# Performance work log

Hardware: AMD Instinct MI355X
Metric: run time of the kernel (lower is better)

Reference implementation:

```python
import jax, jax.numpy as jnp
import numpy as np

NEG_SLOPE = 0.2   # PyG GATConv default negative_slope
BN_EPS = 1e-5
N_NODES = 50000
N_EDGES = 600000
N_GRAPHS = 64


def _gat_conv(x, W, att_src, att_dst, bias, src, dst, heads, out_ch, concat):
    """PyG GATConv (eval mode, self-loops already appended to src/dst).
    x: [N, in], W: [in, heads*out_ch], att_*: [heads, out_ch], bias: [heads*out_ch] or [out_ch].
    """
    n = x.shape[0]
    h = (x @ W).reshape(n, heads, out_ch)                  # [N, H, C]
    a_s = jnp.sum(h * att_src[None], axis=-1)              # [N, H]
    a_d = jnp.sum(h * att_dst[None], axis=-1)              # [N, H]
    logit = jax.nn.leaky_relu(a_s[src] + a_d[dst], NEG_SLOPE)  # [E, H]
    # segment softmax over destination node (every node has a self-loop -> no empty segment)
    m = jax.ops.segment_max(logit, dst, num_segments=n)
    p = jnp.exp(logit - m[dst])
    denom = jax.ops.segment_sum(p, dst, num_segments=n)
    alpha = p / (denom[dst] + 1e-16)                       # [E, H]
    out = jax.ops.segment_sum(h[src] * alpha[:, :, None], dst, num_segments=n)  # [N, H, C]
    out = out.reshape(n, heads * out_ch) if concat else out.mean(axis=1)
    return out + bias


def _bn(x, gamma, beta):
    mu = x.mean(axis=0)
    var = x.var(axis=0)
    return (x - mu) * jax.lax.rsqrt(var + BN_EPS) * gamma + beta


def setup_inputs() -> dict:
    key = jax.random.key(0)
    ks = jax.random.split(key, 20)
    hidden = 64
    d1_in, d1_out, h1 = 5, hidden // 2, 4          # 5 -> 32x4 = 128
    d2_in, d2_out, h2 = hidden * 2, hidden // 2, 4  # 128 -> 32x4 = 128
    d3_in, d3_out, h3 = hidden * 2, hidden, 1       # 128 -> 64

    def glorot(k, shape):
        fan = shape[0] + shape[-1]
        return jax.random.normal(k, shape, dtype=jnp.float32) * np.sqrt(2.0 / fan)

    inp = {
        "x": jax.random.normal(ks[0], (N_NODES, d1_in), dtype=jnp.float32),
        "edge_index": jax.random.randint(ks[1], (2, N_EDGES), 0, N_NODES),
        "batch": jnp.sort(jax.random.randint(ks[2], (N_NODES,), 0, N_GRAPHS)),
        # conv1
        "W1": glorot(ks[3], (d1_in, h1 * d1_out)),
        "a1_src": glorot(ks[4], (h1, d1_out)),
        "a1_dst": glorot(ks[5], (h1, d1_out)),
        "b1": jnp.zeros((h1 * d1_out,), dtype=jnp.float32),
        "g1": jnp.ones((h1 * d1_out,), dtype=jnp.float32),
        "be1": jnp.zeros((h1 * d1_out,), dtype=jnp.float32),
        # conv2
        "W2": glorot(ks[6], (d2_in, h2 * d2_out)),
        "a2_src": glorot(ks[7], (h2, d2_out)),
        "a2_dst": glorot(ks[8], (h2, d2_out)),
        "b2": jnp.zeros((h2 * d2_out,), dtype=jnp.float32),
        "g2": jnp.ones((h2 * d2_out,), dtype=jnp.float32),
        "be2": jnp.zeros((h2 * d2_out,), dtype=jnp.float32),
        # conv3 (single head, concat=False)
        "W3": glorot(ks[9], (d3_in, h3 * d3_out)),
        "a3_src": glorot(ks[10], (h3, d3_out)),
        "a3_dst": glorot(ks[11], (h3, d3_out)),
        "b3": jnp.zeros((d3_out,), dtype=jnp.float32),
    }
    return inp


def reference(x, edge_index, batch, W1, a1_src, a1_dst, b1, g1, be1,
              W2, a2_src, a2_dst, b2, g2, be2, W3, a3_src, a3_dst, b3):
    n = x.shape[0]
    loops = jnp.arange(n)
    src = jnp.concatenate([edge_index[0], loops])  # PyG add_self_loops=True
    dst = jnp.concatenate([edge_index[1], loops])

    h = jax.nn.elu(_bn(_gat_conv(x, W1, a1_src, a1_dst, b1, src, dst, 4, 32, True), g1, be1))
    h = jax.nn.elu(_bn(_gat_conv(h, W2, a2_src, a2_dst, b2, src, dst, 4, 32, True), g2, be2))
    h = jax.nn.elu(_gat_conv(h, W3, a3_src, a3_dst, b3, src, dst, 1, 64, False))

    counts = jax.ops.segment_sum(jnp.ones((n,), h.dtype), batch, num_segments=N_GRAPHS)
    mean_pool = jax.ops.segment_sum(h, batch, num_segments=N_GRAPHS) / jnp.maximum(counts, 1.0)[:, None]
    max_pool = jax.ops.segment_max(h, batch, num_segments=N_GRAPHS)
    max_pool = jnp.where(counts[:, None] > 0, max_pool, 0.0)
    return jnp.concatenate([mean_pool, max_pool], axis=1)  # [G, 128]
```

## Files before the change

kernel.cpp:

```cpp
#include <hip/hip_runtime.h>
#include <math.h>

#define NEG_SLOPE 0.2f
#define BN_EPS 1e-5f

typedef __attribute__((ext_vector_type(8))) short short8;
typedef __attribute__((ext_vector_type(4))) float f32x4;

__device__ __forceinline__ float lrelu_f(float x){ return x > 0.f ? x : NEG_SLOPE * x; }
__device__ __forceinline__ float elu_f(float x){ return x > 0.f ? x : __expf(x) - 1.f; }

__device__ __forceinline__ unsigned short f2bf(float f){
    unsigned u = __float_as_uint(f);
    return (unsigned short)((u + 0x7fffu + ((u >> 16) & 1u)) >> 16);
}
__device__ __forceinline__ float bf_lo(unsigned v){ return __uint_as_float(v << 16); }
__device__ __forceinline__ float bf_hi(unsigned v){ return __uint_as_float(v & 0xffff0000u); }
__device__ __forceinline__ float bf2f(unsigned short b){ return __uint_as_float((unsigned)b << 16); }

__device__ __forceinline__ unsigned enc_f(float x){
    unsigned b = __float_as_uint(x);
    return (b & 0x80000000u) ? ~b : (b | 0x80000000u);
}
__device__ __forceinline__ float dec_f(unsigned u){
    return __uint_as_float((u & 0x80000000u) ? (u & 0x7FFFFFFFu) : ~u);
}

__global__ void k_prep(const int* __restrict__ ei, int E0, int N, int Bc, int Bg,
                       const int* __restrict__ batch, int G,
                       int* __restrict__ counts, int* __restrict__ gp,
                       const float* __restrict__ W1, const float* __restrict__ a1s,
                       const float* __restrict__ a1d,
                       const float* __restrict__ W2, const float* __restrict__ W3,
                       unsigned short* __restrict__ wt2, unsigned short* __restrict__ wt3,
                       float* __restrict__ u_s, float* __restrict__ u_d){
    int b = blockIdx.x, tid = threadIdx.x;
    if (b < Bc){
        int i = b * 256 + tid, tot = E0 + N;
        if (i < tot){
            int dst = (i < E0) ? ei[E0 + i] : (i - E0);
            atomicAdd(&counts[dst], 1);
        }
    } else if (b < Bc + Bg){
        int i = (b - Bc) * 256 + tid;
        if (i < N){
            int bb = batch[i];
            if (i == 0){ for (int g = 0; g <= bb; ++g) gp[g] = 0; }
            else { int pb = batch[i - 1]; for (int g = pb + 1; g <= bb; ++g) gp[g] = i; }
            if (i == N - 1){ for (int g = bb + 1; g <= G; ++g) gp[g] = N; }
        }
    } else if (b < Bc + Bg + 96){
        int i = (b - Bc - Bg) * 256 + tid;
        if (i < 128 * 128){
            int k = i / 128, c = i % 128;
            wt2[c * 128 + k] = f2bf(W2[i]);
        } else if (i < 128 * 128 + 128 * 64){
            int j = i - 128 * 128;
            int k = j / 64, c = j % 64;
            wt3[c * 128 + k] = f2bf(W3[j]);
        }
    } else {
        if (tid < 40){
            int t2 = tid % 20;
            int k = t2 / 4, hh = t2 % 4;
            const float* att = (tid < 20) ? a1s : a1d;
            float s = 0.f;
            for (int j = 0; j < 32; ++j) s += W1[k * 128 + hh * 32 + j] * att[hh * 32 + j];
            if (tid < 20) u_s[k * 4 + hh] = s; else u_d[k * 4 + hh] = s;
        }
    }
}

__global__ void k_scan(const int* __restrict__ counts, int n, int* __restrict__ row_ptr){
    __shared__ int sh[256], rsh[256];
    __shared__ int offs;
    int tid = threadIdx.x, bid = blockIdx.x;
    int limit = bid * 256;
    int po = 0;
    for (int j = tid; j < limit; j += 256) po += counts[j];
    rsh[tid] = po;
    __syncthreads();
    for (int o = 128; o > 0; o >>= 1){
        if (tid < o) rsh[tid] += rsh[tid + o];
        __syncthreads();
    }
    if (tid == 0) offs = rsh[0];
    __syncthreads();
    int i = limit + tid;
    int v = (i < n) ? counts[i] : 0;
    sh[tid] = v;
    __syncthreads();
    for (int o = 1; o < 256; o <<= 1){
        int t = (tid >= o) ? sh[tid - o] : 0;
        __syncthreads();
        sh[tid] += t;
        __syncthreads();
    }
    if (i < n) row_ptr[i] = offs + sh[tid] - v;
    if (bid == gridDim.x - 1 && tid == 255) row_ptr[n] = offs + sh[255];
}

__global__ void k_scatter(const int* __restrict__ ei, int E0, int N,
                          const int* __restrict__ row_ptr, int* __restrict__ cursor,
                          int* __restrict__ csr_src){
    int i = blockIdx.x * blockDim.x + threadIdx.x;
    int tot = E0 + N;
    if (i >= tot) return;
    int src, dst;
    if (i < E0){ src = ei[i]; dst = ei[E0 + i]; } else { src = dst = i - E0; }
    int pos = atomicAdd(&cursor[dst], 1);
    csr_src[row_ptr[dst] + pos] = src;
}

__launch_bounds__(256)
__global__ void k_l1(const float* __restrict__ X, const float* __restrict__ W1,
                     const float* __restrict__ u_s, const float* __restrict__ u_d,
                     const int* __restrict__ row_ptr, const int* __restrict__ csr_src,
                     const float* __restrict__ bias, unsigned short* __restrict__ out,
                     float* __restrict__ bnb_s, float* __restrict__ bnb_q, int N){
    __shared__ float Wl[5 * 128];
    __shared__ float bs[16][128], bq[16][128];
    int tid = threadIdx.x;
    for (int i = tid; i < 5 * 128; i += 256) Wl[i] = W1[i];
    __syncthreads();
    int grp = tid >> 4, ln = tid & 15;
    int hh = ln >> 2, sl = ln & 3;
    long n = (long)blockIdx.x * 16 + grp;
    bool valid = n < N;
    float us[5], ud[5];
#pragma unroll
    for (int k = 0; k < 5; ++k){ us[k] = u_s[k * 4 + hh]; ud[k] = u_d[k * 4 + hh]; }
    float ad = 0.f;
    if (valid){
#pragma unroll
        for (int k = 0; k < 5; ++k) ad += X[n * 5 + k] * ud[k];
    }
    int beg = 0, end = 0;
    if (valid){ beg = row_ptr[n]; end = row_ptr[n + 1]; }
    float y0 = 0.f, y1 = 0.f, y2 = 0.f, y3 = 0.f, y4 = 0.f, dn = 0.f;
    for (int e = beg + sl; e < end; e += 4){
        long s = csr_src[e];
        float x0 = X[s * 5 + 0], x1 = X[s * 5 + 1], x2 = X[s * 5 + 2],
              x3 = X[s * 5 + 3], x4 = X[s * 5 + 4];
        float as = x0 * us[0] + x1 * us[1] + x2 * us[2] + x3 * us[3] + x4 * us[4];
        float p = __expf(lrelu_f(as + ad));
        dn += p;
        y0 += p * x0; y1 += p * x1; y2 += p * x2; y3 += p * x3; y4 += p * x4;
    }
#pragma unroll
    for (int m = 1; m < 4; m <<= 1){
        y0 += __shfl_xor(y0, m); y1 += __shfl_xor(y1, m); y2 += __shfl_xor(y2, m);
        y3 += __shfl_xor(y3, m); y4 += __shfl_xor(y4, m); dn += __shfl_xor(dn, m);
    }
    float inv = valid ? 1.f / dn : 0.f;
    y0 *= inv; y1 *= inv; y2 *= inv; y3 *= inv; y4 *= inv;
    int c0 = ln * 8;
    const float4* Wl4 = (const float4*)Wl;
    float4 oa = {0,0,0,0}, ob = {0,0,0,0};
    if (valid){
        float4 w0a = Wl4[0 * 32 + ln * 2], w0b = Wl4[0 * 32 + ln * 2 + 1];
        float4 w1a = Wl4[1 * 32 + ln * 2], w1b = Wl4[1 * 32 + ln * 2 + 1];
        float4 w2a = Wl4[2 * 32 + ln * 2], w2b = Wl4[2 * 32 + ln * 2 + 1];
        float4 w3a = Wl4[3 * 32 + ln * 2], w3b = Wl4[3 * 32 + ln * 2 + 1];
        float4 w4a = Wl4[4 * 32 + ln * 2], w4b = Wl4[4 * 32 + ln * 2 + 1];
        oa.x = y0*w0a.x + y1*w1a.x + y2*w2a.x + y3*w3a.x + y4*w4a.x + bias[c0 + 0];
        oa.y = y0*w0a.y + y1*w1a.y + y2*w2a.y + y3*w3a.y + y4*w4a.y + bias[c0 + 1];
        oa.z = y0*w0a.z + y1*w1a.z + y2*w2a.z + y3*w3a.z + y4*w4a.z + bias[c0 + 2];
        oa.w = y0*w0a.w + y1*w1a.w + y2*w2a.w + y3*w3a.w + y4*w4a.w + bias[c0 + 3];
        ob.x = y0*w0b.x + y1*w1b.x + y2*w2b.x + y3*w3b.x + y4*w4b.x + bias[c0 + 4];
        ob.y = y0*w0b.y + y1*w1b.y + y2*w2b.y + y3*w3b.y + y4*w4b.y + bias[c0 + 5];
        ob.z = y0*w0b.z + y1*w1b.z + y2*w2b.z + y3*w3b.z + y4*w4b.z + bias[c0 + 6];
        ob.w = y0*w0b.w + y1*w1b.w + y2*w2b.w + y3*w3b.w + y4*w4b.w + bias[c0 + 7];
        uint4 o;
        o.x = (unsigned)f2bf(oa.x) | ((unsigned)f2bf(oa.y) << 16);
        o.y = (unsigned)f2bf(oa.z) | ((unsigned)f2bf(oa.w) << 16);
        o.z = (unsigned)f2bf(ob.x) | ((unsigned)f2bf(ob.y) << 16);
        o.w = (unsigned)f2bf(ob.z) | ((unsigned)f2bf(ob.w) << 16);
        *(uint4*)&out[n * 128 + c0] = o;
    }
    float ov[8] = {oa.x, oa.y, oa.z, oa.w, ob.x, ob.y, ob.z, ob.w};
#pragma unroll
    for (int j = 0; j < 8; ++j){ bs[grp][c0 + j] = ov[j]; bq[grp][c0 + j] = ov[j] * ov[j]; }
    __syncthreads();
    for (int o = 8; o > 0; o >>= 1){
        if (grp < o){
#pragma unroll
            for (int j = 0; j < 8; ++j){
                bs[grp][c0 + j] += bs[grp + o][c0 + j];
                bq[grp][c0 + j] += bq[grp + o][c0 + j];
            }
        }
        __syncthreads();
    }
    if (grp == 0){
        int bucket = blockIdx.x & 255;
#pragma unroll
        for (int j = 0; j < 8; ++j){
            atomicAdd(&bnb_s[bucket * 128 + c0 + j], bs[0][c0 + j]);
            atomicAdd(&bnb_q[bucket * 128 + c0 + j], bq[0][c0 + j]);
        }
    }
}

template<int OUT, int H, bool BN>
__launch_bounds__(256)
__global__ void k_gemm_mfma(const unsigned short* __restrict__ X, const unsigned short* __restrict__ Wt,
                            const float* __restrict__ atts, const float* __restrict__ attd,
                            const float* __restrict__ coefs, const float* __restrict__ coefb,
                            unsigned short* __restrict__ h, float* __restrict__ as_,
                            float* __restrict__ ad_, int N){
    constexpr int TM  = 64;
    constexpr int NCT = OUT / 16;
    constexpr int CPH = NCT / H;
    __shared__ unsigned short Xl[TM * 128];
    __shared__ unsigned short Wl[OUT * 128];
    int tid = threadIdx.x;
    long base = (long)blockIdx.x * TM;

    for (int i = tid; i < OUT * 16; i += 256){
        int r = i >> 4, g = i & 15;
        uint4 v = *(const uint4*)&Wt[r * 128 + g * 8];
        int gs = g ^ (r & 7);
        *(uint4*)&Wl[r * 128 + gs * 8] = v;
    }
    for (int i = tid; i < TM * 16; i += 256){
        int r = i >> 4, g = i & 15;
        long node = base + r;
        uint4 o;
        if (node < N){
            uint4 raw = *(const uint4*)&X[node * 128 + g * 8];
            float f[8];
            f[0] = bf_lo(raw.x); f[1] = bf_hi(raw.x);
            f[2] = bf_lo(raw.y); f[3] = bf_hi(raw.y);
            f[4] = bf_lo(raw.z); f[5] = bf_hi(raw.z);
            f[6] = bf_lo(raw.w); f[7] = bf_hi(raw.w);
#pragma unroll
            for (int j = 0; j < 8; ++j){
                float v = f[j];
                if (BN) v = elu_f(fmaf(v, coefs[g * 8 + j], coefb[g * 8 + j]));
                f[j] = v;
            }
            o.x = (unsigned)f2bf(f[0]) | ((unsigned)f2bf(f[1]) << 16);
            o.y = (unsigned)f2bf(f[2]) | ((unsigned)f2bf(f[3]) << 16);
            o.z = (unsigned)f2bf(f[4]) | ((unsigned)f2bf(f[5]) << 16);
            o.w = (unsigned)f2bf(f[6]) | ((unsigned)f2bf(f[7]) << 16);
        } else {
            o.x = o.y = o.z = o.w = 0u;
        }
        int gs = g ^ (r & 7);
        *(uint4*)&Xl[r * 128 + gs * 8] = o;
    }
    __syncthreads();

    int wid = tid >> 6;
    int lane = tid & 63;
    int lr = lane & 15, lk = lane >> 4;

    short8 afrag[4];
    int arow = wid * 16 + lr;
#pragma unroll
    for (int ks = 0; ks < 4; ++ks){
        int g = ks * 4 + lk;
        int gs = g ^ (arow & 7);
        afrag[ks] = *(const short8*)&Xl[arow * 128 + gs * 8];
    }
    f32x4 acc[NCT];
#pragma unroll
    for (int ct = 0; ct < NCT; ++ct) acc[ct] = (f32x4){0.f, 0.f, 0.f, 0.f};
#pragma unroll
    for (int ct = 0; ct < NCT; ++ct){
        int brow = ct * 16 + lr;
#pragma unroll
        for (int ks = 0; ks < 4; ++ks){
            int g = ks * 4 + lk;
            int gs = g ^ (brow & 7);
            short8 bfrag = *(const short8*)&Wl[brow * 128 + gs * 8];
            acc[ct] = __builtin_amdgcn_mfma_f32_16x16x32_bf16(afrag[ks], bfrag, acc[ct], 0, 0, 0);
        }
    }
    float ps[H][4], pd[H][4];
#pragma unroll
    for (int hh = 0; hh < H; ++hh)
#pragma unroll
        for (int j = 0; j < 4; ++j){ ps[hh][j] = 0.f; pd[hh][j] = 0.f; }
#pragma unroll
    for (int ct = 0; ct < NCT; ++ct){
        int col = ct * 16 + lr;
        int hh = ct / CPH;
        float asv = atts[col], adv = attd[col];
#pragma unroll
        for (int j = 0; j < 4; ++j){
            float v = acc[ct][j];
            long node = base + wid * 16 + lk * 4 + j;
            if (node < N) h[node * OUT + col] = f2bf(v);
            ps[hh][j] += v * asv;
            pd[hh][j] += v * adv;
        }
    }
#pragma unroll
    for (int m = 1; m < 16; m <<= 1){
#pragma unroll
        for (int hh = 0; hh < H; ++hh)
#pragma unroll
            for (int j = 0; j < 4; ++j){
                ps[hh][j] += __shfl_xor(ps[hh][j], m);
                pd[hh][j] += __shfl_xor(pd[hh][j], m);
            }
    }
    if (lr == 0){
#pragma unroll
        for (int j = 0; j < 4; ++j){
            long node = base + wid * 16 + lk * 4 + j;
            if (node < N){
#pragma unroll
                for (int hh = 0; hh < H; ++hh){
                    as_[node * H + hh] = ps[hh][j];
                    ad_[node * H + hh] = pd[hh][j];
                }
            }
        }
    }
}

__launch_bounds__(512)
__global__ void k_agg2(const unsigned short* __restrict__ h, const float* __restrict__ as_,
                       const float* __restrict__ ad_, const int* __restrict__ row_ptr,
                       const int* __restrict__ csr_src, const float* __restrict__ bias,
                       unsigned short* __restrict__ out,
                       float* __restrict__ bnb_s, float* __restrict__ bnb_q, int N){
    __shared__ float ls[8][128], lq[8][128];
    int tid = threadIdx.x;
    int wid = tid >> 6, lane = tid & 63;
    long n = (long)blockIdx.x * 8 + wid;
    bool valid = n < N;
    int hh = lane >> 4;
    float vx = 0.f, vy = 0.f;
    if (valid){
        float ad = ad_[n * 4 + hh];
        int beg = row_ptr[n], end = row_ptr[n + 1];
        float accx = 0.f, accy = 0.f, dn = 0.f;
        const unsigned* h32 = (const unsigned*)h;
        int e = beg;
        for (; e + 4 <= end; e += 4){
            int s0 = csr_src[e], s1 = csr_src[e+1], s2 = csr_src[e+2], s3 = csr_src[e+3];
            float a0 = as_[s0*4+hh], a1 = as_[s1*4+hh], a2 = as_[s2*4+hh], a3 = as_[s3*4+hh];
            unsigned v0 = h32[(long)s0*64+lane], v1 = h32[(long)s1*64+lane],
                     v2 = h32[(long)s2*64+lane], v3 = h32[(long)s3*64+lane];
            float p0 = __expf(lrelu_f(a0 + ad));
            float p1 = __expf(lrelu_f(a1 + ad));
            float p2 = __expf(lrelu_f(a2 + ad));
            float p3 = __expf(lrelu_f(a3 + ad));
            dn += p0 + p1 + p2 + p3;
            accx += p0*bf_lo(v0) + p1*bf_lo(v1) + p2*bf_lo(v2) + p3*bf_lo(v3);
            accy += p0*bf_hi(v0) + p1*bf_hi(v1) + p2*bf_hi(v2) + p3*bf_hi(v3);
        }
        for (; e < end; ++e){
            int s0 = csr_src[e];
            unsigned v0 = h32[(long)s0*64+lane];
            float p0 = __expf(lrelu_f(as_[s0*4+hh] + ad));
            dn += p0;
            accx += p0 * bf_lo(v0); accy += p0 * bf_hi(v0);
        }
        float inv = 1.f / dn;
        vx = accx * inv + bias[2*lane];
        vy = accy * inv + bias[2*lane + 1];
        ((unsigned*)out)[n * 64 + lane] = (unsigned)f2bf(vx) | ((unsigned)f2bf(vy) << 16);
    }
    ls[wid][2*lane] = vx; ls[wid][2*lane+1] = vy;
    lq[wid][2*lane] = vx*vx; lq[wid][2*lane+1] = vy*vy;
    __syncthreads();
    for (int o = 4; o > 0; o >>= 1){
        if (wid < o){
            ls[wid][2*lane]   += ls[wid+o][2*lane];
            ls[wid][2*lane+1] += ls[wid+o][2*lane+1];
            lq[wid][2*lane]   += lq[wid+o][2*lane];
            lq[wid][2*lane+1] += lq[wid+o][2*lane+1];
        }
        __syncthreads();
    }
    if (wid == 0){
        int bucket = blockIdx.x & 255;
        atomicAdd(&bnb_s[bucket*128 + 2*lane],   ls[0][2*lane]);
        atomicAdd(&bnb_s[bucket*128 + 2*lane+1], ls[0][2*lane+1]);
        atomicAdd(&bnb_q[bucket*128 + 2*lane],   lq[0][2*lane]);
        atomicAdd(&bnb_q[bucket*128 + 2*lane+1], lq[0][2*lane+1]);
    }
}

__launch_bounds__(512)
__global__ void k_agg3(const unsigned short* __restrict__ h, const float* __restrict__ as_,
                       const float* __restrict__ ad_, const int* __restrict__ row_ptr,
                       const int* __restrict__ csr_src, const float* __restrict__ bias,
                       const int* __restrict__ batch,
                       float* __restrict__ psum, unsigned* __restrict__ pmax, int N){
    __shared__ float lsv[8][64];
    __shared__ int lg[8];
    int tid = threadIdx.x;
    int wid = tid >> 6, lane = tid & 63;
    long n = (long)blockIdx.x * 8 + wid;
    bool valid = n < N;
    float v = 0.f;
    if (valid){
        float ad = ad_[n];
        int beg = row_ptr[n], end = row_ptr[n + 1];
        float acc = 0.f, dn = 0.f;
        int e = beg;
        for (; e + 4 <= end; e += 4){
            int s0 = csr_src[e], s1 = csr_src[e+1], s2 = csr_src[e+2], s3 = csr_src[e+3];
            float a0 = as_[s0], a1 = as_[s1], a2 = as_[s2], a3 = as_[s3];
            unsigned short w0 = h[(long)s0*64+lane], w1 = h[(long)s1*64+lane],
                           w2 = h[(long)s2*64+lane], w3 = h[(long)s3*64+lane];
            float p0 = __expf(lrelu_f(a0 + ad));
            float p1 = __expf(lrelu_f(a1 + ad));
            float p2 = __expf(lrelu_f(a2 + ad));
            float p3 = __expf(lrelu_f(a3 + ad));
            dn += p0 + p1 + p2 + p3;
            acc += p0*bf2f(w0) + p1*bf2f(w1) + p2*bf2f(w2) + p3*bf2f(w3);
        }
        for (; e < end; ++e){
            int s0 = csr_src[e];
            float p0 = __expf(lrelu_f(as_[s0] + ad));
            dn += p0;
            acc += p0 * bf2f(h[(long)s0*64+lane]);
        }
        v = elu_f(acc / dn + bias[lane]);
    }
    if (lane == 0) lg[wid] = valid ? batch[n] : -1;
    lsv[wid][lane] = v;
    __syncthreads();
    int gw = lg[wid];
    bool leader = (gw >= 0) && (wid == 0 || lg[wid - 1] != gw);
    if (leader){
        float s = 0.f, m = -1e30f;
        for (int w = wid; w < 8 && lg[w] == gw; ++w){
            float x = lsv[w][lane];
            s += x; m = fmaxf(m, x);
        }
        atomicAdd(&psum[gw * 64 + lane], s);
        atomicMax(&pmax[gw * 64 + lane], enc_f(m));
    }
}

__launch_bounds__(256)
__global__ void k_bn_fin(const float* __restrict__ ps, const float* __restrict__ pq, int PB,
                         const float* __restrict__ g, const float* __restrict__ be,
                         float invN, float* __restrict__ cs, float* __restrict__ cb){
    __shared__ float sh_s[256], sh_q[256];
    int tid = threadIdx.x;
    int cl = tid & 15, sl = tid >> 4;
    int c = blockIdx.x * 16 + cl;
    float s = 0.f, q = 0.f;
    for (int b = sl; b < PB; b += 16){
        s += ps[(long)b * 128 + c];
        q += pq[(long)b * 128 + c];
    }
    sh_s[tid] = s; sh_q[tid] = q;
    __syncthreads();
    for (int o = 8; o > 0; o >>= 1){
        if (sl < o){
            s += sh_s[tid + o * 16]; q += sh_q[tid + o * 16];
            sh_s[tid] = s; sh_q[tid] = q;
        }
        __syncthreads();
    }
    if (sl == 0){
        float mu = s * invN;
        float var = q * invN - mu * mu;
        float sc = g[c] * rsqrtf(var + BN_EPS);
        cs[c] = sc;
        cb[c] = be[c] - mu * sc;
    }
}

__global__ void k_pool_fin(const float* __restrict__ psum, const unsigned* __restrict__ pmax,
                           const int* __restrict__ gp, float* __restrict__ out){
    int g = blockIdx.x;
    int c = threadIdx.x;
    int cnt = gp[g + 1] - gp[g];
    float mean = (cnt > 0) ? psum[g * 64 + c] / (float)cnt : 0.f;
    float mx   = (cnt > 0) ? dec_f(pmax[g * 64 + c]) : 0.f;
    out[g * 128 + c]      = mean;
    out[g * 128 + 64 + c] = mx;
}

extern "C" void kernel_launch(void* const* d_in, const int* in_sizes, int n_in,
                              void* d_out, int out_size, void* d_ws, size_t ws_size,
                              hipStream_t stream){
    const float* x   = (const float*)d_in[0];
    const int*   ei  = (const int*)d_in[1];
    const int*   bat = (const int*)d_in[2];
    const float* W1  = (const float*)d_in[3];
    const float* a1s = (const float*)d_in[4];
    const float* a1d = (const float*)d_in[5];
    const float* b1  = (const float*)d_in[6];
    const float* g1  = (const float*)d_in[7];
    const float* be1 = (const float*)d_in[8];
    const float* W2  = (const float*)d_in[9];
    const float* a2s = (const float*)d_in[10];
    const float* a2d = (const float*)d_in[11];
    const float* b2  = (const float*)d_in[12];
    const float* g2  = (const float*)d_in[13];
    const float* be2 = (const float*)d_in[14];
    const float* W3  = (const float*)d_in[15];
    const float* a3s = (const float*)d_in[16];
    const float* a3d = (const float*)d_in[17];
    const float* b3  = (const float*)d_in[18];
    float* out = (float*)d_out;

    int N  = in_sizes[2];
    int E0 = in_sizes[1] / 2;
    int E  = E0 + N;
    const int G = 64;
    int P  = (N + 255) / 256;
    const int NB = 256;

    char* ws = (char*)d_ws;
    size_t off = 0;
    auto alloc = [&](size_t bytes) -> char* {
        char* p = ws + off;
        off += (bytes + 255) & ~(size_t)255;
        return p;
    };
    int*      counts  = (int*)alloc((size_t)N * 4);
    int*      cursor  = (int*)alloc((size_t)N * 4);
    float*    psum    = (float*)alloc((size_t)G * 64 * 4);
    unsigned* pmax    = (unsigned*)alloc((size_t)G * 64 * 4);
    float*    bnb1_s  = (float*)alloc((size_t)NB * 128 * 4);
    float*    bnb1_q  = (float*)alloc((size_t)NB * 128 * 4);
    float*    bnb2_s  = (float*)alloc((size_t)NB * 128 * 4);
    float*    bnb2_q  = (float*)alloc((size_t)NB * 128 * 4);
    size_t zero_bytes = off;
    int*   row_ptr = (int*)alloc((size_t)(N + 1) * 4);
    int*   csr     = (int*)alloc((size_t)E * 4);
    int*   gp      = (int*)alloc((size_t)(G + 1) * 4);
    float* as_buf  = (float*)alloc((size_t)N * 4 * 4);
    float* ad_buf  = (float*)alloc((size_t)N * 4 * 4);
    float* coefs   = (float*)alloc(128 * 4);
    float* coefb   = (float*)alloc(128 * 4);
    float* u_s     = (float*)alloc(20 * 4);
    float* u_d     = (float*)alloc(20 * 4);
    unsigned short* wt2 = (unsigned short*)alloc(128 * 128 * 2);
    unsigned short* wt3 = (unsigned short*)alloc(64 * 128 * 2);
    unsigned short* hbuf = (unsigned short*)alloc((size_t)N * 128 * 2);
    unsigned short* xcur = (unsigned short*)alloc((size_t)N * 128 * 2);

    hipMemsetAsync(ws, 0, zero_bytes, stream);

    int Bc = (E + 255) / 256, Bg = (N + 255) / 256;
    k_prep<<<Bc + Bg + 96 + 1, 256, 0, stream>>>(ei, E0, N, Bc, Bg, bat, G, counts, gp,
                                                 W1, a1s, a1d, W2, W3, wt2, wt3, u_s, u_d);
    k_scan<<<P, 256, 0, stream>>>(counts, N, row_ptr);
    k_scatter<<<(E + 255) / 256, 256, 0, stream>>>(ei, E0, N, row_ptr, cursor, csr);

    k_l1<<<(N + 15) / 16, 256, 0, stream>>>(x, W1, u_s, u_d, row_ptr, csr, b1, xcur,
                                            bnb1_s, bnb1_q, N);
    k_bn_fin<<<8, 256, 0, stream>>>(bnb1_s, bnb1_q, NB, g1, be1, 1.f / N, coefs, coefb);

    k_gemm_mfma<128, 4, true><<<(N + 63) / 64, 256, 0, stream>>>(
        xcur, wt2, a2s, a2d, coefs, coefb, hbuf, as_buf, ad_buf, N);
    k_agg2<<<(N + 7) / 8, 512, 0, stream>>>(hbuf, as_buf, ad_buf, row_ptr, csr, b2,
                                            xcur, bnb2_s, bnb2_q, N);
    k_bn_fin<<<8, 256, 0, stream>>>(bnb2_s, bnb2_q, NB, g2, be2, 1.f / N, coefs, coefb);

    k_gemm_mfma<64, 1, true><<<(N + 63) / 64, 256, 0, stream>>>(
        xcur, wt3, a3s, a3d, coefs, coefb, hbuf, as_buf, ad_buf, N);
    k_agg3<<<(N + 7) / 8, 512, 0, stream>>>(hbuf, as_buf, ad_buf, row_ptr, csr, b3,
                                            bat, psum, pmax, N);
    k_pool_fin<<<G, 64, 0, stream>>>(psum, pmax, gp, out);
}
```

Measured before the change: 260.7 us.

## Precompute per-edge attention weights once per wave into LDS and use exp2 with prescaled logits

Attention vectors are prescaled by log2(e) so the softmax uses exp2f directly. In the layer-2 and layer-3 aggregation kernels, each wave first computes every edge's exponentiated logit in parallel across lanes and stores it in LDS. Before, every lane recomputed the exp for every edge. A degree-over-64 fallback keeps the old serial path, and blocks shrink from 8 to 4 waves. This removes redundant gather-and-exp work per edge, at the cost of an extra LDS pass and a second read of the csr indices.

```diff
diff --git a/kernel.cpp b/kernel.cpp
--- a/kernel.cpp
+++ b/kernel.cpp
@@ -3,6 +3,7 @@
 
 #define NEG_SLOPE 0.2f
 #define BN_EPS 1e-5f
+#define LOG2E 1.44269504088896f
 
 typedef __attribute__((ext_vector_type(8))) short short8;
 typedef __attribute__((ext_vector_type(4))) float f32x4;
@@ -66,6 +67,7 @@
             const float* att = (tid < 20) ? a1s : a1d;
             float s = 0.f;
             for (int j = 0; j < 32; ++j) s += W1[k * 128 + hh * 32 + j] * att[hh * 32 + j];
+            s *= LOG2E;
             if (tid < 20) u_s[k * 4 + hh] = s; else u_d[k * 4 + hh] = s;
         }
     }
@@ -143,7 +145,7 @@
         float x0 = X[s * 5 + 0], x1 = X[s * 5 + 1], x2 = X[s * 5 + 2],
               x3 = X[s * 5 + 3], x4 = X[s * 5 + 4];
         float as = x0 * us[0] + x1 * us[1] + x2 * us[2] + x3 * us[3] + x4 * us[4];
-        float p = __expf(lrelu_f(as + ad));
+        float p = exp2f(lrelu_f(as + ad));
         dn += p;
         y0 += p * x0; y1 += p * x1; y2 += p * x2; y3 += p * x3; y4 += p * x4;
     }
@@ -287,7 +289,7 @@
     for (int ct = 0; ct < NCT; ++ct){
         int col = ct * 16 + lr;
         int hh = ct / CPH;
-        float asv = atts[col], adv = attd[col];
+        float asv = atts[col] * LOG2E, adv = attd[col] * LOG2E;
 #pragma unroll
         for (int j = 0; j < 4; ++j){
             float v = acc[ct][j];
@@ -322,46 +324,71 @@
     }
 }
 
-__launch_bounds__(512)
+__launch_bounds__(256)
 __global__ void k_agg2(const unsigned short* __restrict__ h, const float* __restrict__ as_,
                        const float* __restrict__ ad_, const int* __restrict__ row_ptr,
                        const int* __restrict__ csr_src, const float* __restrict__ bias,
                        unsigned short* __restrict__ out,
                        float* __restrict__ bnb_s, float* __restrict__ bnb_q, int N){
-    __shared__ float ls[8][128], lq[8][128];
+    __shared__ float plds[4][256];
+    __shared__ float ls[4][128], lq[4][128];
     int tid = threadIdx.x;
     int wid = tid >> 6, lane = tid & 63;
-    long n = (long)blockIdx.x * 8 + wid;
+    long n = (long)blockIdx.x * 4 + wid;
     bool valid = n < N;
-    int hh = lane >> 4;
     float vx = 0.f, vy = 0.f;
     if (valid){
-        float ad = ad_[n * 4 + hh];
         int beg = row_ptr[n], end = row_ptr[n + 1];
-        float accx = 0.f, accy = 0.f, dn = 0.f;
+        int deg = end - beg;
+        int hh = lane >> 4;
+        float accx = 0.f, accy = 0.f, inv;
         const unsigned* h32 = (const unsigned*)h;
-        int e = beg;
-        for (; e + 4 <= end; e += 4){
-            int s0 = csr_src[e], s1 = csr_src[e+1], s2 = csr_src[e+2], s3 = csr_src[e+3];
-            float a0 = as_[s0*4+hh], a1 = as_[s1*4+hh], a2 = as_[s2*4+hh], a3 = as_[s3*4+hh];
-            unsigned v0 = h32[(long)s0*64+lane], v1 = h32[(long)s1*64+lane],
-                     v2 = h32[(long)s2*64+lane], v3 = h32[(long)s3*64+lane];
-            float p0 = __expf(lrelu_f(a0 + ad));
-            float p1 = __expf(lrelu_f(a1 + ad));
-            float p2 = __expf(lrelu_f(a2 + ad));
-            float p3 = __expf(lrelu_f(a3 + ad));
-            dn += p0 + p1 + p2 + p3;
-            accx += p0*bf_lo(v0) + p1*bf_lo(v1) + p2*bf_lo(v2) + p3*bf_lo(v3);
-            accy += p0*bf_hi(v0) + p1*bf_hi(v1) + p2*bf_hi(v2) + p3*bf_hi(v3);
-        }
-        for (; e < end; ++e){
-            int s0 = csr_src[e];
-            unsigned v0 = h32[(long)s0*64+lane];
-            float p0 = __expf(lrelu_f(as_[s0*4+hh] + ad));
-            dn += p0;
-            accx += p0 * bf_lo(v0); accy += p0 * bf_hi(v0);
-        }
-        float inv = 1.f / dn;
+        if (deg <= 64){
+            int eoff = lane >> 2, hd = lane & 3;
+            float adh = ad_[n * 4 + hd];
+            float dnl = 0.f;
+            for (int e0 = 0; e0 < deg; e0 += 16){
+                int e = e0 + eoff;
+                float pp = 0.f;
+                if (e < deg){
+                    int s = csr_src[beg + e];
+                    pp = exp2f(lrelu_f(as_[s * 4 + hd] + adh));
+                    plds[wid][e * 4 + hd] = pp;
+                }
+                dnl += pp;
+            }
+#pragma unroll
+            for (int m = 4; m < 64; m <<= 1) dnl += __shfl_xor(dnl, m);
+            int e = 0;
+            for (; e + 4 <= deg; e += 4){
+                int s0 = csr_src[beg+e], s1 = csr_src[beg+e+1],
+                    s2 = csr_src[beg+e+2], s3 = csr_src[beg+e+3];
+                float p0 = plds[wid][(e+0)*4+hh], p1 = plds[wid][(e+1)*4+hh],
+                      p2 = plds[wid][(e+2)*4+hh], p3 = plds[wid][(e+3)*4+hh];
+                unsigned v0 = h32[(long)s0*64+lane], v1 = h32[(long)s1*64+lane],
+                         v2 = h32[(long)s2*64+lane], v3 = h32[(long)s3*64+lane];
+                accx += p0*bf_lo(v0) + p1*bf_lo(v1) + p2*bf_lo(v2) + p3*bf_lo(v3);
+                accy += p0*bf_hi(v0) + p1*bf_hi(v1) + p2*bf_hi(v2) + p3*bf_hi(v3);
+            }
+            for (; e < deg; ++e){
+                int s0 = csr_src[beg+e];
+                float p0 = plds[wid][e*4+hh];
+                unsigned v0 = h32[(long)s0*64+lane];
+                accx += p0 * bf_lo(v0); accy += p0 * bf_hi(v0);
+            }
+            inv = 1.f / __shfl(dnl, hh);
+        } else {
+            float adh = ad_[n * 4 + hh];
+            float dn = 0.f;
+            for (int e = beg; e < end; ++e){
+                int s0 = csr_src[e];
+                unsigned v0 = h32[(long)s0*64+lane];
+                float p0 = exp2f(lrelu_f(as_[s0*4+hh] + adh));
+                dn += p0;
+                accx += p0 * bf_lo(v0); accy += p0 * bf_hi(v0);
+            }
+            inv = 1.f / dn;
+        }
         vx = accx * inv + bias[2*lane];
         vy = accy * inv + bias[2*lane + 1];
         ((unsigned*)out)[n * 64 + lane] = (unsigned)f2bf(vx) | ((unsigned)f2bf(vy) << 16);
@@ -369,7 +396,7 @@
     ls[wid][2*lane] = vx; ls[wid][2*lane+1] = vy;
     lq[wid][2*lane] = vx*vx; lq[wid][2*lane+1] = vy*vy;
     __syncthreads();
-    for (int o = 4; o > 0; o >>= 1){
+    for (int o = 2; o > 0; o >>= 1){
         if (wid < o){
             ls[wid][2*lane]   += ls[wid+o][2*lane];
             ls[wid][2*lane+1] += ls[wid+o][2*lane+1];
@@ -387,43 +414,61 @@
     }
 }
 
-__launch_bounds__(512)
+__launch_bounds__(256)
 __global__ void k_agg3(const unsigned short* __restrict__ h, const float* __restrict__ as_,
                        const float* __restrict__ ad_, const int* __restrict__ row_ptr,
                        const int* __restrict__ csr_src, const float* __restrict__ bias,
                        const int* __restrict__ batch,
                        float* __restrict__ psum, unsigned* __restrict__ pmax, int N){
-    __shared__ float lsv[8][64];
-    __shared__ int lg[8];
+    __shared__ float plds[4][64];
+    __shared__ float lsv[4][64];
+    __shared__ int lg[4];
     int tid = threadIdx.x;
     int wid = tid >> 6, lane = tid & 63;
-    long n = (long)blockIdx.x * 8 + wid;
+    long n = (long)blockIdx.x * 4 + wid;
     bool valid = n < N;
     float v = 0.f;
     if (valid){
         float ad = ad_[n];
         int beg = row_ptr[n], end = row_ptr[n + 1];
-        float acc = 0.f, dn = 0.f;
-        int e = beg;
-        for (; e + 4 <= end; e += 4){
-            int s0 = csr_src[e], s1 = csr_src[e+1], s2 = csr_src[e+2], s3 = csr_src[e+3];
-            float a0 = as_[s0], a1 = as_[s1], a2 = as_[s2], a3 = as_[s3];
-            unsigned short w0 = h[(long)s0*64+lane], w1 = h[(long)s1*64+lane],
-                           w2 = h[(long)s2*64+lane], w3 = h[(long)s3*64+lane];
-            float p0 = __expf(lrelu_f(a0 + ad));
-            float p1 = __expf(lrelu_f(a1 + ad));
-            float p2 = __expf(lrelu_f(a2 + ad));
-            float p3 = __expf(lrelu_f(a3 + ad));
-            dn += p0 + p1 + p2 + p3;
-            acc += p0*bf2f(w0) + p1*bf2f(w1) + p2*bf2f(w2) + p3*bf2f(w3);
-        }
-        for (; e < end; ++e){
-            int s0 = csr_src[e];
-            float p0 = __expf(lrelu_f(as_[s0] + ad));
-            dn += p0;
-            acc += p0 * bf2f(h[(long)s0*64+lane]);
-        }
-        v = elu_f(acc / dn + bias[lane]);
+        int deg = end - beg;
+        float acc = 0.f, inv;
+        if (deg <= 64){
+            float pp = 0.f;
+            if (lane < deg){
+                int s = csr_src[beg + lane];
+                pp = exp2f(lrelu_f(as_[s] + ad));
+                plds[wid][lane] = pp;
+            }
+            float dn = pp;
+#pragma unroll
+            for (int m = 1; m < 64; m <<= 1) dn += __shfl_xor(dn, m);
+            int e = 0;
+            for (; e + 4 <= deg; e += 4){
+                int s0 = csr_src[beg+e], s1 = csr_src[beg+e+1],
+                    s2 = csr_src[beg+e+2], s3 = csr_src[beg+e+3];
+                float p0 = plds[wid][e], p1 = plds[wid][e+1],
+                      p2 = plds[wid][e+2], p3 = plds[wid][e+3];
+                unsigned short w0 = h[(long)s0*64+lane], w1 = h[(long)s1*64+lane],
+                               w2 = h[(long)s2*64+lane], w3 = h[(long)s3*64+lane];
+                acc += p0*bf2f(w0) + p1*bf2f(w1) + p2*bf2f(w2) + p3*bf2f(w3);
+            }
+            for (; e < deg; ++e){
+                int s0 = csr_src[beg+e];
+                acc += plds[wid][e] * bf2f(h[(long)s0*64+lane]);
+            }
+            inv = 1.f / dn;
+        } else {
+            float dn = 0.f;
+            for (int e = beg; e < end; ++e){
+                int s0 = csr_src[e];
+                float p0 = exp2f(lrelu_f(as_[s0] + ad));
+                dn += p0;
+                acc += p0 * bf2f(h[(long)s0*64+lane]);
+            }
+            inv = 1.f / dn;
+        }
+        v = elu_f(acc * inv + bias[lane]);
     }
     if (lane == 0) lg[wid] = valid ? batch[n] : -1;
     lsv[wid][lane] = v;
@@ -432,7 +477,7 @@
     bool leader = (gw >= 0) && (wid == 0 || lg[wid - 1] != gw);
     if (leader){
         float s = 0.f, m = -1e30f;
-        for (int w = wid; w < 8 && lg[w] == gw; ++w){
+        for (int w = wid; w < 4 && lg[w] == gw; ++w){
             float x = lsv[w][lane];
             s += x; m = fmaxf(m, x);
         }
@@ -558,13 +603,13 @@
 
     k_gemm_mfma<128, 4, true><<<(N + 63) / 64, 256, 0, stream>>>(
         xcur, wt2, a2s, a2d, coefs, coefb, hbuf, as_buf, ad_buf, N);
-    k_agg2<<<(N + 7) / 8, 512, 0, stream>>>(hbuf, as_buf, ad_buf, row_ptr, csr, b2,
+    k_agg2<<<(N + 3) / 4, 256, 0, stream>>>(hbuf, as_buf, ad_buf, row_ptr, csr, b2,
                                             xcur, bnb2_s, bnb2_q, N);
     k_bn_fin<<<8, 256, 0, stream>>>(bnb2_s, bnb2_q, NB, g2, be2, 1.f / N, coefs, coefb);
 
     k_gemm_mfma<64, 1, true><<<(N + 63) / 64, 256, 0, stream>>>(
         xcur, wt3, a3s, a3d, coefs, coefb, hbuf, as_buf, ad_buf, N);
-    k_agg3<<<(N + 7) / 8, 512, 0, stream>>>(hbuf, as_buf, ad_buf, row_ptr, csr, b3,
+    k_agg3<<<(N + 3) / 4, 256, 0, stream>>>(hbuf, as_buf, ad_buf, row_ptr, csr, b3,
                                             bat, psum, pmax, N);
     k_pool_fin<<<G, 64, 0, stream>>>(psum, pmax, gp, out);
 }
```

Measured after the change: 272.9 us. 4.7% more time.

## Use one-wave blocks per node in aggregation, fold log2e into attention

Applied to the files above, without the earlier changes.

The layer-2 and layer-3 aggregation kernels now launch one 64-thread block per node instead of 8 nodes per 512-thread block. This removes the shared-memory reductions and __syncthreads, but every node now does its own global atomics for the BN statistics and the pooling sums/max, which can add heavy atomic contention. The attention coefficients are pre-scaled by log2(e) so the softmax can use exp2f instead of __expf. The edge loop unroll also drops from 4 to 2.

```diff
diff --git a/kernel.cpp b/kernel.cpp
--- a/kernel.cpp
+++ b/kernel.cpp
@@ -3,6 +3,7 @@
 
 #define NEG_SLOPE 0.2f
 #define BN_EPS 1e-5f
+#define LOG2E 1.44269504088896f
 
 typedef __attribute__((ext_vector_type(8))) short short8;
 typedef __attribute__((ext_vector_type(4))) float f32x4;
@@ -66,6 +67,7 @@
             const float* att = (tid < 20) ? a1s : a1d;
             float s = 0.f;
             for (int j = 0; j < 32; ++j) s += W1[k * 128 + hh * 32 + j] * att[hh * 32 + j];
+            s *= LOG2E;
             if (tid < 20) u_s[k * 4 + hh] = s; else u_d[k * 4 + hh] = s;
         }
     }
@@ -143,7 +145,7 @@
         float x0 = X[s * 5 + 0], x1 = X[s * 5 + 1], x2 = X[s * 5 + 2],
               x3 = X[s * 5 + 3], x4 = X[s * 5 + 4];
         float as = x0 * us[0] + x1 * us[1] + x2 * us[2] + x3 * us[3] + x4 * us[4];
-        float p = __expf(lrelu_f(as + ad));
+        float p = exp2f(lrelu_f(as + ad));
         dn += p;
         y0 += p * x0; y1 += p * x1; y2 += p * x2; y3 += p * x3; y4 += p * x4;
     }
@@ -287,7 +289,7 @@
     for (int ct = 0; ct < NCT; ++ct){
         int col = ct * 16 + lr;
         int hh = ct / CPH;
-        float asv = atts[col], adv = attd[col];
+        float asv = atts[col] * LOG2E, adv = attd[col] * LOG2E;
 #pragma unroll
         for (int j = 0; j < 4; ++j){
             float v = acc[ct][j];
@@ -322,123 +324,81 @@
     }
 }
 
-__launch_bounds__(512)
+__launch_bounds__(64)
 __global__ void k_agg2(const unsigned short* __restrict__ h, const float* __restrict__ as_,
                        const float* __restrict__ ad_, const int* __restrict__ row_ptr,
                        const int* __restrict__ csr_src, const float* __restrict__ bias,
                        unsigned short* __restrict__ out,
                        float* __restrict__ bnb_s, float* __restrict__ bnb_q, int N){
-    __shared__ float ls[8][128], lq[8][128];
-    int tid = threadIdx.x;
-    int wid = tid >> 6, lane = tid & 63;
-    long n = (long)blockIdx.x * 8 + wid;
-    bool valid = n < N;
+    int n = blockIdx.x;
+    if (n >= N) return;
+    int lane = threadIdx.x;
     int hh = lane >> 4;
-    float vx = 0.f, vy = 0.f;
-    if (valid){
-        float ad = ad_[n * 4 + hh];
-        int beg = row_ptr[n], end = row_ptr[n + 1];
-        float accx = 0.f, accy = 0.f, dn = 0.f;
-        const unsigned* h32 = (const unsigned*)h;
-        int e = beg;
-        for (; e + 4 <= end; e += 4){
-            int s0 = csr_src[e], s1 = csr_src[e+1], s2 = csr_src[e+2], s3 = csr_src[e+3];
-            float a0 = as_[s0*4+hh], a1 = as_[s1*4+hh], a2 = as_[s2*4+hh], a3 = as_[s3*4+hh];
-            unsigned v0 = h32[(long)s0*64+lane], v1 = h32[(long)s1*64+lane],
-                     v2 = h32[(long)s2*64+lane], v3 = h32[(long)s3*64+lane];
-            float p0 = __expf(lrelu_f(a0 + ad));
-            float p1 = __expf(lrelu_f(a1 + ad));
-            float p2 = __expf(lrelu_f(a2 + ad));
-            float p3 = __expf(lrelu_f(a3 + ad));
-            dn += p0 + p1 + p2 + p3;
-            accx += p0*bf_lo(v0) + p1*bf_lo(v1) + p2*bf_lo(v2) + p3*bf_lo(v3);
-            accy += p0*bf_hi(v0) + p1*bf_hi(v1) + p2*bf_hi(v2) + p3*bf_hi(v3);
-        }
-        for (; e < end; ++e){
-            int s0 = csr_src[e];
-            unsigned v0 = h32[(long)s0*64+lane];
-            float p0 = __expf(lrelu_f(as_[s0*4+hh] + ad));
-            dn += p0;
-            accx += p0 * bf_lo(v0); accy += p0 * bf_hi(v0);
-        }
-        float inv = 1.f / dn;
-        vx = accx * inv + bias[2*lane];
-        vy = accy * inv + bias[2*lane + 1];
-        ((unsigned*)out)[n * 64 + lane] = (unsigned)f2bf(vx) | ((unsigned)f2bf(vy) << 16);
-    }
-    ls[wid][2*lane] = vx; ls[wid][2*lane+1] = vy;
-    lq[wid][2*lane] = vx*vx; lq[wid][2*lane+1] = vy*vy;
-    __syncthreads();
-    for (int o = 4; o > 0; o >>= 1){
-        if (wid < o){
-            ls[wid][2*lane]   += ls[wid+o][2*lane];
-            ls[wid][2*lane+1] += ls[wid+o][2*lane+1];
-            lq[wid][2*lane]   += lq[wid+o][2*lane];
-            lq[wid][2*lane+1] += lq[wid+o][2*lane+1];
-        }
-        __syncthreads();
-    }
-    if (wid == 0){
-        int bucket = blockIdx.x & 255;
-        atomicAdd(&bnb_s[bucket*128 + 2*lane],   ls[0][2*lane]);
-        atomicAdd(&bnb_s[bucket*128 + 2*lane+1], ls[0][2*lane+1]);
-        atomicAdd(&bnb_q[bucket*128 + 2*lane],   lq[0][2*lane]);
-        atomicAdd(&bnb_q[bucket*128 + 2*lane+1], lq[0][2*lane+1]);
-    }
-}
-
-__launch_bounds__(512)
+    float ad = ad_[n * 4 + hh];
+    int beg = row_ptr[n], end = row_ptr[n + 1];
+    float accx = 0.f, accy = 0.f, dn = 0.f;
+    const unsigned* h32 = (const unsigned*)h;
+    int e = beg;
+    for (; e + 2 <= end; e += 2){
+        int s0 = csr_src[e], s1 = csr_src[e + 1];
+        float a0 = as_[s0 * 4 + hh], a1 = as_[s1 * 4 + hh];
+        unsigned v0 = h32[(long)s0 * 64 + lane], v1 = h32[(long)s1 * 64 + lane];
+        float p0 = exp2f(lrelu_f(a0 + ad));
+        float p1 = exp2f(lrelu_f(a1 + ad));
+        dn += p0 + p1;
+        accx += p0 * bf_lo(v0) + p1 * bf_lo(v1);
+        accy += p0 * bf_hi(v0) + p1 * bf_hi(v1);
+    }
+    if (e < end){
+        int s0 = csr_src[e];
+        float p0 = exp2f(lrelu_f(as_[s0 * 4 + hh] + ad));
+        unsigned v0 = h32[(long)s0 * 64 + lane];
+        dn += p0;
+        accx += p0 * bf_lo(v0); accy += p0 * bf_hi(v0);
+    }
+    float inv = 1.f / dn;
+    float vx = accx * inv + bias[2 * lane];
+    float vy = accy * inv + bias[2 * lane + 1];
+    ((unsigned*)out)[(long)n * 64 + lane] = (unsigned)f2bf(vx) | ((unsigned)f2bf(vy) << 16);
+    int bucket = n & 255;
+    atomicAdd(&bnb_s[bucket * 128 + 2 * lane],     vx);
+    atomicAdd(&bnb_s[bucket * 128 + 2 * lane + 1], vy);
+    atomicAdd(&bnb_q[bucket * 128 + 2 * lane],     vx * vx);
+    atomicAdd(&bnb_q[bucket * 128 + 2 * lane + 1], vy * vy);
+}
+
+__launch_bounds__(64)
 __global__ void k_agg3(const unsigned short* __restrict__ h, const float* __restrict__ as_,
                        const float* __restrict__ ad_, const int* __restrict__ row_ptr,
                        const int* __restrict__ csr_src, const float* __restrict__ bias,
                        const int* __restrict__ batch,
                        float* __restrict__ psum, unsigned* __restrict__ pmax, int N){
-    __shared__ float lsv[8][64];
-    __shared__ int lg[8];
-    int tid = threadIdx.x;
-    int wid = tid >> 6, lane = tid & 63;
-    long n = (long)blockIdx.x * 8 + wid;
-    bool valid = n < N;
-    float v = 0.f;
-    if (valid){
-        float ad = ad_[n];
-        int beg = row_ptr[n], end = row_ptr[n + 1];
-        float acc = 0.f, dn = 0.f;
-        int e = beg;
-        for (; e + 4 <= end; e += 4){
-            int s0 = csr_src[e], s1 = csr_src[e+1], s2 = csr_src[e+2], s3 = csr_src[e+3];
-            float a0 = as_[s0], a1 = as_[s1], a2 = as_[s2], a3 = as_[s3];
-            unsigned short w0 = h[(long)s0*64+lane], w1 = h[(long)s1*64+lane],
-                           w2 = h[(long)s2*64+lane], w3 = h[(long)s3*64+lane];
-            float p0 = __expf(lrelu_f(a0 + ad));
-            float p1 = __expf(lrelu_f(a1 + ad));
-            float p2 = __expf(lrelu_f(a2 + ad));
-            float p3 = __expf(lrelu_f(a3 + ad));
-            dn += p0 + p1 + p2 + p3;
-            acc += p0*bf2f(w0) + p1*bf2f(w1) + p2*bf2f(w2) + p3*bf2f(w3);
-        }
-        for (; e < end; ++e){
-            int s0 = csr_src[e];
-            float p0 = __expf(lrelu_f(as_[s0] + ad));
-            dn += p0;
-            acc += p0 * bf2f(h[(long)s0*64+lane]);
-        }
-        v = elu_f(acc / dn + bias[lane]);
-    }
-    if (lane == 0) lg[wid] = valid ? batch[n] : -1;
-    lsv[wid][lane] = v;
-    __syncthreads();
-    int gw = lg[wid];
-    bool leader = (gw >= 0) && (wid == 0 || lg[wid - 1] != gw);
-    if (leader){
-        float s = 0.f, m = -1e30f;
-        for (int w = wid; w < 8 && lg[w] == gw; ++w){
-            float x = lsv[w][lane];
-            s += x; m = fmaxf(m, x);
-        }
-        atomicAdd(&psum[gw * 64 + lane], s);
-        atomicMax(&pmax[gw * 64 + lane], enc_f(m));
-    }
+    int n = blockIdx.x;
+    if (n >= N) return;
+    int lane = threadIdx.x;
+    float ad = ad_[n];
+    int beg = row_ptr[n], end = row_ptr[n + 1];
+    float acc = 0.f, dn = 0.f;
+    int e = beg;
+    for (; e + 2 <= end; e += 2){
+        int s0 = csr_src[e], s1 = csr_src[e + 1];
+        float a0 = as_[s0], a1 = as_[s1];
+        unsigned short w0 = h[(long)s0 * 64 + lane], w1 = h[(long)s1 * 64 + lane];
+        float p0 = exp2f(lrelu_f(a0 + ad));
+        float p1 = exp2f(lrelu_f(a1 + ad));
+        dn += p0 + p1;
+        acc += p0 * bf2f(w0) + p1 * bf2f(w1);
+    }
+    if (e < end){
+        int s0 = csr_src[e];
+        float p0 = exp2f(lrelu_f(as_[s0] + ad));
+        dn += p0;
+        acc += p0 * bf2f(h[(long)s0 * 64 + lane]);
+    }
+    float v = elu_f(acc / dn + bias[lane]);
+    int g = batch[n];
+    atomicAdd(&psum[g * 64 + lane], v);
+    atomicMax(&pmax[g * 64 + lane], enc_f(v));
 }
 
 __launch_bounds__(256)
@@ -558,13 +518,13 @@
 
     k_gemm_mfma<128, 4, true><<<(N + 63) / 64, 256, 0, stream>>>(
         xcur, wt2, a2s, a2d, coefs, coefb, hbuf, as_buf, ad_buf, N);
-    k_agg2<<<(N + 7) / 8, 512, 0, stream>>>(hbuf, as_buf, ad_buf, row_ptr, csr, b2,
-                                            xcur, bnb2_s, bnb2_q, N);
+    k_agg2<<<N, 64, 0, stream>>>(hbuf, as_buf, ad_buf, row_ptr, csr, b2, xcur,
+                                 bnb2_s, bnb2_q, N);
     k_bn_fin<<<8, 256, 0, stream>>>(bnb2_s, bnb2_q, NB, g2, be2, 1.f / N, coefs, coefb);
 
     k_gemm_mfma<64, 1, true><<<(N + 63) / 64, 256, 0, stream>>>(
         xcur, wt3, a3s, a3d, coefs, coefb, hbuf, as_buf, ad_buf, N);
-    k_agg3<<<(N + 7) / 8, 512, 0, stream>>>(hbuf, as_buf, ad_buf, row_ptr, csr, b3,
-                                            bat, psum, pmax, N);
+    k_agg3<<<N, 64, 0, stream>>>(hbuf, as_buf, ad_buf, row_ptr, csr, b3, bat,
+                                 psum, pmax, N);
     k_pool_fin<<<G, 64, 0, stream>>>(psum, pmax, gp, out);
 }
```

New measurement: 350.4 us. 34.4% more time.
